# Kernel optimization log

Hardware: AMD Instinct MI355X
Metric: run time of the kernel (lower is better)

## Reference

```python
import jax, jax.numpy as jnp
import numpy as np

S, D, H, E = 4096, 1024, 16, 64  # seq_len, embed_dim, n_heads, head_size


def setup_inputs() -> dict:
    key = jax.random.key(0)
    ks = jax.random.split(key, 8)
    s_d = 1.0 / np.sqrt(D).astype(np.float32)
    return {
        "x": jax.random.normal(ks[0], (S, D), jnp.float32),
        # per-head Q/K/V projections (no bias), stacked over heads: [H, D, E]
        "Wk": jax.random.normal(ks[1], (H, D, E), jnp.float32) * s_d,
        "Wq": jax.random.normal(ks[2], (H, D, E), jnp.float32) * s_d,
        "Wv": jax.random.normal(ks[3], (H, D, E), jnp.float32) * s_d,
        # output projection Dense(D) with bias
        "Wo": jax.random.normal(ks[4], (H * E, D), jnp.float32) * (1.0 / np.sqrt(H * E).astype(np.float32)),
        "bo": jnp.zeros((D,), jnp.float32),
        # MLP: Dense(4D) -> gelu -> Dense(D), both with bias
        "W1": jax.random.normal(ks[5], (D, 4 * D), jnp.float32) * s_d,
        "b1": jnp.zeros((4 * D,), jnp.float32),
        "W2": jax.random.normal(ks[6], (4 * D, D), jnp.float32) * (1.0 / np.sqrt(4 * D).astype(np.float32)),
        "b2": jnp.zeros((D,), jnp.float32),
    }


def _attention(x, Wk, Wq, Wv):
    # per-head projections, vectorized over heads (original loops in Python)
    k = jnp.einsum('sd,hde->hse', x, Wk)
    q = jnp.einsum('sd,hde->hse', x, Wq)
    v = jnp.einsum('sd,hde->hse', x, Wv)
    # NOTE: original computes keys @ queries.T -> scores[i, j] = k_i . q_j
    scores = jnp.einsum('hse,hte->hst', k, q) / jnp.sqrt(jnp.float32(E))
    mask = jnp.tril(jnp.ones((x.shape[0], x.shape[0]), dtype=bool))  # [S, S]
    w = jax.nn.softmax(jnp.where(mask, scores, -jnp.inf), axis=-1)   # [H, S, S]
    out = jnp.einsum('hst,hte->hse', w, v)                            # [H, S, E]
    # concatenate heads along feature axis (head 0 first, matching the loop)
    return out.transpose(1, 0, 2).reshape(x.shape[0], -1)             # [S, H*E]


def reference(x, Wk, Wq, Wv, Wo, bo, W1, b1, W2, b2):
    x = x + _attention(x, Wk, Wq, Wv) @ Wo + bo
    h = jax.nn.gelu(x @ W1 + b1, approximate=True)  # flax default gelu (tanh approx)
    return x + h @ W2 + b2
```

## Files before the change

### kernel.cpp

```cpp
#include <hip/hip_runtime.h>

typedef __attribute__((ext_vector_type(8))) short s16x8;
typedef __attribute__((ext_vector_type(4))) short s16x4;
typedef __attribute__((ext_vector_type(4))) float f32x4;


__device__ __forceinline__ unsigned short f2bf(float f) {
    union { float f; unsigned u; } v; v.f = f;
    unsigned r = v.u + 0x7FFFu + ((v.u >> 16) & 1u);
    return (unsigned short)(r >> 16);
}

__device__ __forceinline__ unsigned cvt_pk_bf16(float lo, float hi) {
    unsigned r;
    asm("v_cvt_pk_bf16_f32 %0, %1, %2" : "=v"(r) : "v"(lo), "v"(hi));
    return r;
}

__device__ __forceinline__ float exp2_fast(float x) {
    float r;
    asm("v_exp_f32 %0, %1" : "=v"(r) : "v"(x));
    return r;
}

__device__ __forceinline__ float gelu_tanh(float x) {
    float u = 0.7978845608028654f * (x + 0.044715f * x * x * x);
    float au = fabsf(u);
    float t = 1.f - 2.f / (__expf(2.f * au) + 1.f);
    t = (u < 0.f) ? -t : t;
    return 0.5f * x * (1.f + t);
}

__device__ __forceinline__ void load_lds16(const void* g, void* l) {
    __builtin_amdgcn_global_load_lds(
        (const __attribute__((address_space(1))) void*)g,
        (__attribute__((address_space(3))) void*)l, 16, 0, 0);
}

__device__ __forceinline__ void xcd_remap(int& bx, int& by) {
    const int gx = gridDim.x;
    const int nwg = gx * gridDim.y;
    const int id = by * gx + bx;
    const int nid = (id & 7) * (nwg >> 3) + (id >> 3);
    bx = nid % gx; by = nid / gx;
}


__global__ void convert_bf16_k(const float* __restrict__ in,
                               unsigned short* __restrict__ out, int n) {
    int i = (blockIdx.x * blockDim.x + threadIdx.x) * 4;
    if (i >= n) return;
    float4 v = *(const float4*)(in + i);
    ushort4 o;
    o.x = f2bf(v.x); o.y = f2bf(v.y); o.z = f2bf(v.z); o.w = f2bf(v.w);
    *(ushort4*)(out + i) = o;
}

__global__ void transpose_k(const float* __restrict__ in,
                            unsigned short* __restrict__ out, int R, int C) {
    __shared__ float tile[32][33];
    const int b = blockIdx.z;
    const int c0 = blockIdx.x * 32, r0 = blockIdx.y * 32;
    const float* inb = in + (size_t)b * R * C;
    unsigned short* outb = out + (size_t)b * R * C;
    const int tx = threadIdx.x, ty = threadIdx.y;
    #pragma unroll
    for (int i = 0; i < 4; ++i)
        tile[ty + i*8][tx] = inb[(size_t)(r0 + ty + i*8) * C + c0 + tx];
    __syncthreads();
    #pragma unroll
    for (int i = 0; i < 4; ++i)
        outb[(size_t)(c0 + ty + i*8) * R + r0 + tx] = f2bf(tile[tx][ty + i*8]);
}

template<int EPI>
__global__ __launch_bounds__(256) void gemm_bt(
    const unsigned short* __restrict__ A,
    const unsigned short* __restrict__ BT,
    const float* __restrict__ bias,
    const float* __restrict__ resid,
    float* __restrict__ Cf,
    unsigned short* __restrict__ Cb,
    int M, int N, int K)
{
    __shared__ unsigned short As[3][128 * 32];
    __shared__ unsigned short Bs[3][128 * 32];
    const int tid = threadIdx.x;
    const int w  = tid >> 6, l = tid & 63;
    const int wr = w >> 1,  wc = w & 1;
    const int lg = l >> 4,  ll = l & 15;
    int bx = blockIdx.x, by = blockIdx.y;
    xcd_remap(bx, by);
    const int m0 = by * 128, n0 = bx * 128;

    const int srow = w * 16 + (l >> 2);
    const int scol = (((l & 3) ^ ((l >> 2) & 3))) * 8;

    f32x4 acc[4][4] = {};

    auto stage = [&](int buf, int k0) {
        #pragma unroll
        for (int i = 0; i < 2; ++i) {
            load_lds16(A  + (size_t)(m0 + srow + i*64) * K + k0 + scol,
                       (char*)As[buf] + i*4096 + w*1024);
            load_lds16(BT + (size_t)(n0 + srow + i*64) * K + k0 + scol,
                       (char*)Bs[buf] + i*4096 + w*1024);
        }
    };

    const int nsteps = K >> 5;
    stage(0, 0); stage(1, 32);
    int buf = 0;
    for (int s = 0; s < nsteps; ++s) {
        if (s + 1 < nsteps) asm volatile("s_waitcnt vmcnt(4)" ::: "memory");
        else                asm volatile("s_waitcnt vmcnt(0)" ::: "memory");
        __builtin_amdgcn_s_barrier();
        s16x8 a[4], b[4];
        #pragma unroll
        for (int m = 0; m < 4; ++m) {
            const int row = wr*64 + m*16 + ll;
            a[m] = *(const s16x8*)&As[buf][row * 32 + ((lg ^ (ll & 3)) * 8)];
        }
        #pragma unroll
        for (int n = 0; n < 4; ++n) {
            const int row = wc*64 + n*16 + ll;
            b[n] = *(const s16x8*)&Bs[buf][row * 32 + ((lg ^ (ll & 3)) * 8)];
        }
        int bnext = buf + 2; if (bnext >= 3) bnext -= 3;
        if (s + 2 < nsteps) stage(bnext, (s + 2) << 5);
        __builtin_amdgcn_s_setprio(1);
        #pragma unroll
        for (int m = 0; m < 4; ++m)
            #pragma unroll
            for (int n = 0; n < 4; ++n)
                acc[m][n] = __builtin_amdgcn_mfma_f32_16x16x32_bf16(a[m], b[n], acc[m][n], 0, 0, 0);
        __builtin_amdgcn_s_setprio(0);
        buf = (buf == 2) ? 0 : buf + 1;
    }

    #pragma unroll
    for (int m = 0; m < 4; ++m) {
        #pragma unroll
        for (int n = 0; n < 4; ++n) {
            const int col = n0 + wc*64 + n*16 + ll;
            #pragma unroll
            for (int r = 0; r < 4; ++r) {
                const int row = m0 + wr*64 + m*16 + lg*4 + r;
                float v = acc[m][n][r];
                if constexpr (EPI == 2) v = gelu_tanh(v + bias[col]);
                if constexpr (EPI == 4) v *= (col < 1024) ? 0.1803368801f : 1.0f;
                Cb[(size_t)row * N + col] = f2bf(v);
            }
        }
    }
}

template<int EPI>
__global__ __launch_bounds__(256) void gemm_bt64(
    const unsigned short* __restrict__ A,
    const unsigned short* __restrict__ BT,
    const float* __restrict__ bias,
    const float* __restrict__ resid,
    float* __restrict__ Cf,
    unsigned short* __restrict__ Cb,
    int M, int N, int K)
{
    __shared__ unsigned short As[4][128 * 32];
    __shared__ unsigned short Bs[4][64 * 32];
    const int tid = threadIdx.x;
    const int w  = tid >> 6, l = tid & 63;
    const int lg = l >> 4,  ll = l & 15;
    int bx = blockIdx.x, by = blockIdx.y;
    xcd_remap(bx, by);
    const int m0 = by * 128, n0 = bx * 64;

    const int srowA = w * 16 + (l >> 2);
    const int scolA = (((l & 3) ^ ((l >> 2) & 3))) * 8;
    const int srowB = tid >> 2;
    const int scolB = (((tid & 3) ^ ((tid >> 2) & 3))) * 8;

    f32x4 acc[2][4] = {};

    auto stage = [&](int buf, int k0) {
        #pragma unroll
        for (int i = 0; i < 2; ++i)
            load_lds16(A + (size_t)(m0 + srowA + i*64) * K + k0 + scolA,
                       (char*)As[buf] + i*4096 + w*1024);
        load_lds16(BT + (size_t)(n0 + srowB) * K + k0 + scolB,
                   (char*)Bs[buf] + w*1024);
    };

    const int nsteps = K >> 5;
    stage(0, 0); stage(1, 32); stage(2, 64);
    int buf = 0;
    for (int s = 0; s < nsteps; ++s) {
        const int rem = nsteps - 1 - s;
        if (rem >= 2)      asm volatile("s_waitcnt vmcnt(6)" ::: "memory");
        else if (rem == 1) asm volatile("s_waitcnt vmcnt(3)" ::: "memory");
        else               asm volatile("s_waitcnt vmcnt(0)" ::: "memory");
        __builtin_amdgcn_s_barrier();
        s16x8 a[2], b[4];
        #pragma unroll
        for (int m = 0; m < 2; ++m) {
            const int row = w*32 + m*16 + ll;
            a[m] = *(const s16x8*)&As[buf][row * 32 + ((lg ^ (ll & 3)) * 8)];
        }
        #pragma unroll
        for (int n = 0; n < 4; ++n) {
            const int row = n*16 + ll;
            b[n] = *(const s16x8*)&Bs[buf][row * 32 + ((lg ^ (ll & 3)) * 8)];
        }
        int bnext = buf + 3; if (bnext >= 4) bnext -= 4;
        if (s + 3 < nsteps) stage(bnext, (s + 3) << 5);
        __builtin_amdgcn_s_setprio(1);
        #pragma unroll
        for (int m = 0; m < 2; ++m)
            #pragma unroll
            for (int n = 0; n < 4; ++n)
                acc[m][n] = __builtin_amdgcn_mfma_f32_16x16x32_bf16(a[m], b[n], acc[m][n], 0, 0, 0);
        __builtin_amdgcn_s_setprio(0);
        buf = (buf + 1) & 3;
    }

    #pragma unroll
    for (int m = 0; m < 2; ++m) {
        #pragma unroll
        for (int n = 0; n < 4; ++n) {
            const int col = n0 + n*16 + ll;
            #pragma unroll
            for (int r = 0; r < 4; ++r) {
                const int row = m0 + w*32 + m*16 + lg*4 + r;
                float v = acc[m][n][r];
                if constexpr (EPI == 1 || EPI == 3) v += bias[col] + resid[(size_t)row * N + col];
                if constexpr (EPI != 3)
                    Cb[(size_t)row * N + col] = f2bf(v);
                if constexpr (EPI == 1 || EPI == 3)
                    Cf[(size_t)row * N + col] = v;
            }
        }
    }
}

__global__ __launch_bounds__(256) void attn_k(
    const unsigned short* __restrict__ Rq,
    const unsigned short* __restrict__ Ck,
    const unsigned short* __restrict__ Vt,
    unsigned short* __restrict__ Out)
{
    __shared__ unsigned short Ks[3][64 * 64];
    __shared__ unsigned short Vs[3][64 * 64];

    const int bx = blockIdx.x;
    const int h  = bx & 15;
    const int sb = 63 - (bx >> 4);
    const int TOTAL = sb + 1;

    const int tid = threadIdx.x;
    const int w = tid >> 6, l = tid & 63;
    const int lg = l >> 4, ll = l & 15;

    const int gsrc  = ((l & 7) ^ (l >> 3)) * 8;
    const int kOff0 = (w*16 +     (l >> 3)) * 2048 + h*64 + gsrc;
    const int kOff1 = (w*16 + 8 + (l >> 3)) * 2048 + h*64 + gsrc;
    const int vOff0 = (h*64 + w*16 +     (l >> 3)) * 4096 + gsrc;
    const int vOff1 = (h*64 + w*16 + 8 + (l >> 3)) * 4096 + gsrc;
    const int ldsOff = w * 2048;

    int qkoff[4][2];
    #pragma unroll
    for (int jj = 0; jj < 4; ++jj) {
        const int row = jj*16 + ll, r7 = row & 7;
        qkoff[jj][0] = row*128 + ((lg)     ^ r7) * 16;
        qkoff[jj][1] = row*128 + ((4 + lg) ^ r7) * 16;
    }
    int pvoff[4][2][2];
    #pragma unroll
    for (int n = 0; n < 4; ++n) {
        const int row = n*16 + ll, r7 = row & 7;
        #pragma unroll
        for (int c = 0; c < 2; ++c) {
            const int gl = (c*4     + (lg >> 1)) ^ r7;
            const int gh = (c*4 + 2 + (lg >> 1)) ^ r7;
            pvoff[n][c][0] = row*128 + gl*16 + (lg & 1)*8;
            pvoff[n][c][1] = row*128 + gh*16 + (lg & 1)*8;
        }
    }

    auto stage = [&](int t, int buf) {
        const unsigned short* qsrc = Ck + (size_t)t * 131072;
        const unsigned short* vsrc = Vt + t * 64;
        char* kd = (char*)Ks[buf] + ldsOff;
        char* vd = (char*)Vs[buf] + ldsOff;
        load_lds16(qsrc + kOff0, kd);
        load_lds16(qsrc + kOff1, kd + 1024);
        load_lds16(vsrc + vOff0, vd);
        load_lds16(vsrc + vOff1, vd + 1024);
    };

    const int qg = sb*64 + w*16 + ll;
    const size_t rb = (size_t)qg * 2048 + h*64;
    const s16x8 r0 = *(const s16x8*)&Rq[rb + lg*8];
    const s16x8 r1 = *(const s16x8*)&Rq[rb + 32 + lg*8];

    const short onebf = (short)0x3F80;
    const s16x8 ones = {onebf, onebf, onebf, onebf, onebf, onebf, onebf, onebf};

    f32x4 o[4] = {};
    f32x4 o4 = {};

    stage(0, 0); stage(1 < TOTAL ? 1 : 0, 1);
    int buf = 0;

    for (int t = 0; t < TOTAL; ++t) {
        if (t < TOTAL-1) asm volatile("s_waitcnt vmcnt(4)" ::: "memory");
        else             asm volatile("s_waitcnt vmcnt(0)" ::: "memory");
        __builtin_amdgcn_s_barrier();
        const char* kb = (const char*)Ks[buf];
        const char* vb = (const char*)Vs[buf];
        const bool diag = (t == TOTAL-1);

        f32x4 st[4];
        __builtin_amdgcn_s_setprio(1);
        #pragma unroll
        for (int jj = 0; jj < 4; ++jj) {
            s16x8 k0 = *(const s16x8*)(kb + qkoff[jj][0]);
            s16x8 k1 = *(const s16x8*)(kb + qkoff[jj][1]);
            f32x4 z = {0.f, 0.f, 0.f, 0.f};
            f32x4 t0 = __builtin_amdgcn_mfma_f32_16x16x32_bf16(k0, r0, z, 0, 0, 0);
            st[jj] = __builtin_amdgcn_mfma_f32_16x16x32_bf16(k1, r1, t0, 0, 0, 0);
        }
        __builtin_amdgcn_s_setprio(0);

        int bnext = buf + 2; if (bnext >= 3) bnext -= 3;
        if (t + 2 < TOTAL) stage(t + 2, bnext);

        float p[4][4];
        if (diag) {
            #pragma unroll
            for (int jj = 0; jj < 4; ++jj)
                #pragma unroll
                for (int r = 0; r < 4; ++r) {
                    const int jg = t*64 + jj*16 + lg*4 + r;
                    p[jj][r] = exp2_fast((jg > qg) ? -3e38f : st[jj][r]);
                }
        } else {
            #pragma unroll
            for (int jj = 0; jj < 4; ++jj)
                #pragma unroll
                for (int r = 0; r < 4; ++r)
                    p[jj][r] = exp2_fast(st[jj][r]);
        }

        s16x8 apv[2];
        #pragma unroll
        for (int c = 0; c < 2; ++c) {
            union { unsigned u[4]; s16x8 v; } pk;
            pk.u[0] = cvt_pk_bf16(p[2*c][0],   p[2*c][1]);
            pk.u[1] = cvt_pk_bf16(p[2*c][2],   p[2*c][3]);
            pk.u[2] = cvt_pk_bf16(p[2*c+1][0], p[2*c+1][1]);
            pk.u[3] = cvt_pk_bf16(p[2*c+1][2], p[2*c+1][3]);
            apv[c] = pk.v;
        }
        __builtin_amdgcn_s_setprio(1);
        o4 = __builtin_amdgcn_mfma_f32_16x16x32_bf16(apv[0], ones, o4, 0, 0, 0);
        o4 = __builtin_amdgcn_mfma_f32_16x16x32_bf16(apv[1], ones, o4, 0, 0, 0);
        #pragma unroll
        for (int n = 0; n < 4; ++n) {
            #pragma unroll
            for (int c = 0; c < 2; ++c) {
                s16x4 lo = *(const s16x4*)(vb + pvoff[n][c][0]);
                s16x4 hi = *(const s16x4*)(vb + pvoff[n][c][1]);
                union { s16x4 h2[2]; s16x8 v; } u;
                u.h2[0] = lo; u.h2[1] = hi;
                o[n] = __builtin_amdgcn_mfma_f32_16x16x32_bf16(apv[c], u.v, o[n], 0, 0, 0);
            }
        }
        __builtin_amdgcn_s_setprio(0);

        buf = (buf == 2) ? 0 : buf + 1;
    }

    #pragma unroll
    for (int r = 0; r < 4; ++r) {
        const float li = 1.f / o4[r];
        const size_t orow = (size_t)(sb*64 + w*16 + lg*4 + r) * 1024 + h * 64;
        #pragma unroll
        for (int n = 0; n < 4; ++n)
            Out[orow + n*16 + ll] = f2bf(o[n][r] * li);
    }
}


extern "C" void kernel_launch(void* const* d_in, const int* in_sizes, int n_in,
                              void* d_out, int out_size, void* d_ws, size_t ws_size,
                              hipStream_t stream) {
    const float* x  = (const float*)d_in[0];
    const float* Wk = (const float*)d_in[1];
    const float* Wq = (const float*)d_in[2];
    const float* Wv = (const float*)d_in[3];
    const float* Wo = (const float*)d_in[4];
    const float* bo = (const float*)d_in[5];
    const float* W1 = (const float*)d_in[6];
    const float* b1 = (const float*)d_in[7];
    const float* W2 = (const float*)d_in[8];
    const float* b2 = (const float*)d_in[9];
    float* out = (float*)d_out;

    char* ws = (char*)d_ws;
    unsigned short* x_bf  = (unsigned short*)(ws);
    unsigned short* WqkT  = (unsigned short*)(ws + (8u  << 20));
    unsigned short* WvT   = (unsigned short*)(ws + (12u << 20));
    unsigned short* WoT   = (unsigned short*)(ws + (14u << 20));
    unsigned short* W1T   = (unsigned short*)(ws + (16u << 20));
    unsigned short* W2T   = (unsigned short*)(ws + (24u << 20));
    unsigned short* QKm   = (unsigned short*)(ws + (32u << 20));
    unsigned short* attn  = (unsigned short*)(ws + (48u << 20));
    unsigned short* Vt    = (unsigned short*)(ws + (56u << 20));
    float*          yf    = (float*)(ws + (64u << 20));
    unsigned short* y_bf  = x_bf;
    unsigned short* h_bf  = QKm;

    dim3 tb(32, 8);
    convert_bf16_k<<<4096, 256, 0, stream>>>(x, x_bf, 4096 * 1024);
    transpose_k<<<dim3(2, 32, 16),  tb, 0, stream>>>(Wq, WqkT,               1024, 64);
    transpose_k<<<dim3(2, 32, 16),  tb, 0, stream>>>(Wk, WqkT + 1024 * 1024, 1024, 64);
    transpose_k<<<dim3(2, 32, 16),  tb, 0, stream>>>(Wv, WvT, 1024, 64);
    transpose_k<<<dim3(32, 32, 1),  tb, 0, stream>>>(Wo, WoT, 1024, 1024);
    transpose_k<<<dim3(128, 32, 1), tb, 0, stream>>>(W1, W1T, 1024, 4096);
    transpose_k<<<dim3(32, 128, 1), tb, 0, stream>>>(W2, W2T, 4096, 1024);

    gemm_bt<4><<<dim3(16, 32), 256, 0, stream>>>(x_bf, WqkT, nullptr, nullptr, nullptr,
                                                 QKm, 4096, 2048, 1024);
    gemm_bt64<0><<<dim3(64, 8), 256, 0, stream>>>(WvT, x_bf, nullptr, nullptr, nullptr,
                                                  Vt, 1024, 4096, 1024);

    attn_k<<<1024, 256, 0, stream>>>(QKm + 1024 , QKm , Vt, attn);

    gemm_bt64<1><<<dim3(16, 32), 256, 0, stream>>>(attn, WoT, bo, x, yf, y_bf, 4096, 1024, 1024);
    gemm_bt<2><<<dim3(32, 32),   256, 0, stream>>>(y_bf, W1T, b1, nullptr, nullptr, h_bf, 4096, 4096, 1024);
    gemm_bt64<3><<<dim3(16, 32), 256, 0, stream>>>(h_bf, W2T, b2, yf, out, nullptr, 4096, 1024, 4096);
}
```

Baseline: 255.7 us.

## Process 128 query rows per attention block, sharing K/V tiles across two row sets

The attention kernel now handles 128 query rows per block, with each wave taking two 16-row sets, instead of 64 rows per block. Every K/V tile staged into LDS therefore feeds twice as many MFMAs, and the grid is halved to 512 blocks. Each tile also covers more of the diagonal, so the last two tiles are masked. This cuts K/V global loads and per-tile barrier overhead, but it doubles accumulator register pressure and gives fewer blocks for load balance across the causal triangle.

```diff
diff --git a/kernel.cpp b/kernel.cpp
--- a/kernel.cpp
+++ b/kernel.cpp
@@ -252,8 +252,8 @@
 
     const int bx = blockIdx.x;
     const int h  = bx & 15;
-    const int sb = 63 - (bx >> 4);
-    const int TOTAL = sb + 1;
+    const int sb = 31 - (bx >> 4);
+    const int TOTAL = 2*sb + 2;
 
     const int tid = threadIdx.x;
     const int w = tid >> 6, l = tid & 63;
@@ -297,18 +297,23 @@
         load_lds16(vsrc + vOff1, vd + 1024);
     };
 
-    const int qg = sb*64 + w*16 + ll;
-    const size_t rb = (size_t)qg * 2048 + h*64;
-    const s16x8 r0 = *(const s16x8*)&Rq[rb + lg*8];
-    const s16x8 r1 = *(const s16x8*)&Rq[rb + 32 + lg*8];
+    const int row0 = sb*128 + w*32;
+    const int qgA  = row0 + ll;
+    const int qgB  = row0 + 16 + ll;
+    const size_t rbA = (size_t)qgA * 2048 + h*64;
+    const size_t rbB = (size_t)qgB * 2048 + h*64;
+    const s16x8 rA0 = *(const s16x8*)&Rq[rbA + lg*8];
+    const s16x8 rA1 = *(const s16x8*)&Rq[rbA + 32 + lg*8];
+    const s16x8 rB0 = *(const s16x8*)&Rq[rbB + lg*8];
+    const s16x8 rB1 = *(const s16x8*)&Rq[rbB + 32 + lg*8];
 
     const short onebf = (short)0x3F80;
     const s16x8 ones = {onebf, onebf, onebf, onebf, onebf, onebf, onebf, onebf};
 
-    f32x4 o[4] = {};
-    f32x4 o4 = {};
-
-    stage(0, 0); stage(1 < TOTAL ? 1 : 0, 1);
+    f32x4 o[2][4] = {};
+    f32x4 o4[2] = {};
+
+    stage(0, 0); stage(1, 1);
     int buf = 0;
 
     for (int t = 0; t < TOTAL; ++t) {
@@ -317,53 +322,63 @@
         __builtin_amdgcn_s_barrier();
         const char* kb = (const char*)Ks[buf];
         const char* vb = (const char*)Vs[buf];
-        const bool diag = (t == TOTAL-1);
-
-        f32x4 st[4];
+        const bool diag = (t >= 2*sb);
+
+        f32x4 st[2][4];
         __builtin_amdgcn_s_setprio(1);
         #pragma unroll
         for (int jj = 0; jj < 4; ++jj) {
             s16x8 k0 = *(const s16x8*)(kb + qkoff[jj][0]);
             s16x8 k1 = *(const s16x8*)(kb + qkoff[jj][1]);
             f32x4 z = {0.f, 0.f, 0.f, 0.f};
-            f32x4 t0 = __builtin_amdgcn_mfma_f32_16x16x32_bf16(k0, r0, z, 0, 0, 0);
-            st[jj] = __builtin_amdgcn_mfma_f32_16x16x32_bf16(k1, r1, t0, 0, 0, 0);
+            f32x4 ta = __builtin_amdgcn_mfma_f32_16x16x32_bf16(k0, rA0, z, 0, 0, 0);
+            st[0][jj] = __builtin_amdgcn_mfma_f32_16x16x32_bf16(k1, rA1, ta, 0, 0, 0);
+            f32x4 tb = __builtin_amdgcn_mfma_f32_16x16x32_bf16(k0, rB0, z, 0, 0, 0);
+            st[1][jj] = __builtin_amdgcn_mfma_f32_16x16x32_bf16(k1, rB1, tb, 0, 0, 0);
         }
         __builtin_amdgcn_s_setprio(0);
 
         int bnext = buf + 2; if (bnext >= 3) bnext -= 3;
         if (t + 2 < TOTAL) stage(t + 2, bnext);
 
-        float p[4][4];
+        float p[2][4][4];
         if (diag) {
             #pragma unroll
             for (int jj = 0; jj < 4; ++jj)
                 #pragma unroll
                 for (int r = 0; r < 4; ++r) {
                     const int jg = t*64 + jj*16 + lg*4 + r;
-                    p[jj][r] = exp2_fast((jg > qg) ? -3e38f : st[jj][r]);
+                    p[0][jj][r] = exp2_fast((jg > qgA) ? -3e38f : st[0][jj][r]);
+                    p[1][jj][r] = exp2_fast((jg > qgB) ? -3e38f : st[1][jj][r]);
                 }
         } else {
             #pragma unroll
-            for (int jj = 0; jj < 4; ++jj)
+            for (int rs = 0; rs < 2; ++rs)
                 #pragma unroll
-                for (int r = 0; r < 4; ++r)
-                    p[jj][r] = exp2_fast(st[jj][r]);
-        }
-
-        s16x8 apv[2];
-        #pragma unroll
-        for (int c = 0; c < 2; ++c) {
-            union { unsigned u[4]; s16x8 v; } pk;
-            pk.u[0] = cvt_pk_bf16(p[2*c][0],   p[2*c][1]);
-            pk.u[1] = cvt_pk_bf16(p[2*c][2],   p[2*c][3]);
-            pk.u[2] = cvt_pk_bf16(p[2*c+1][0], p[2*c+1][1]);
-            pk.u[3] = cvt_pk_bf16(p[2*c+1][2], p[2*c+1][3]);
-            apv[c] = pk.v;
-        }
+                for (int jj = 0; jj < 4; ++jj)
+                    #pragma unroll
+                    for (int r = 0; r < 4; ++r)
+                        p[rs][jj][r] = exp2_fast(st[rs][jj][r]);
+        }
+
+        s16x8 apv[2][2];
+        #pragma unroll
+        for (int rs = 0; rs < 2; ++rs)
+            #pragma unroll
+            for (int c = 0; c < 2; ++c) {
+                union { unsigned u[4]; s16x8 v; } pk;
+                pk.u[0] = cvt_pk_bf16(p[rs][2*c][0],   p[rs][2*c][1]);
+                pk.u[1] = cvt_pk_bf16(p[rs][2*c][2],   p[rs][2*c][3]);
+                pk.u[2] = cvt_pk_bf16(p[rs][2*c+1][0], p[rs][2*c+1][1]);
+                pk.u[3] = cvt_pk_bf16(p[rs][2*c+1][2], p[rs][2*c+1][3]);
+                apv[rs][c] = pk.v;
+            }
         __builtin_amdgcn_s_setprio(1);
-        o4 = __builtin_amdgcn_mfma_f32_16x16x32_bf16(apv[0], ones, o4, 0, 0, 0);
-        o4 = __builtin_amdgcn_mfma_f32_16x16x32_bf16(apv[1], ones, o4, 0, 0, 0);
+        #pragma unroll
+        for (int rs = 0; rs < 2; ++rs) {
+            o4[rs] = __builtin_amdgcn_mfma_f32_16x16x32_bf16(apv[rs][0], ones, o4[rs], 0, 0, 0);
+            o4[rs] = __builtin_amdgcn_mfma_f32_16x16x32_bf16(apv[rs][1], ones, o4[rs], 0, 0, 0);
+        }
         #pragma unroll
         for (int n = 0; n < 4; ++n) {
             #pragma unroll
@@ -372,7 +387,8 @@
                 s16x4 hi = *(const s16x4*)(vb + pvoff[n][c][1]);
                 union { s16x4 h2[2]; s16x8 v; } u;
                 u.h2[0] = lo; u.h2[1] = hi;
-                o[n] = __builtin_amdgcn_mfma_f32_16x16x32_bf16(apv[c], u.v, o[n], 0, 0, 0);
+                o[0][n] = __builtin_amdgcn_mfma_f32_16x16x32_bf16(apv[0][c], u.v, o[0][n], 0, 0, 0);
+                o[1][n] = __builtin_amdgcn_mfma_f32_16x16x32_bf16(apv[1][c], u.v, o[1][n], 0, 0, 0);
             }
         }
         __builtin_amdgcn_s_setprio(0);
@@ -381,13 +397,15 @@
     }
 
     #pragma unroll
-    for (int r = 0; r < 4; ++r) {
-        const float li = 1.f / o4[r];
-        const size_t orow = (size_t)(sb*64 + w*16 + lg*4 + r) * 1024 + h * 64;
-        #pragma unroll
-        for (int n = 0; n < 4; ++n)
-            Out[orow + n*16 + ll] = f2bf(o[n][r] * li);
-    }
+    for (int rs = 0; rs < 2; ++rs)
+        #pragma unroll
+        for (int r = 0; r < 4; ++r) {
+            const float li = 1.f / o4[rs][r];
+            const size_t orow = (size_t)(row0 + rs*16 + lg*4 + r) * 1024 + h * 64;
+            #pragma unroll
+            for (int n = 0; n < 4; ++n)
+                Out[orow + n*16 + ll] = f2bf(o[rs][n][r] * li);
+        }
 }
 
 
@@ -434,7 +452,7 @@
     gemm_bt64<0><<<dim3(64, 8), 256, 0, stream>>>(WvT, x_bf, nullptr, nullptr, nullptr,
                                                   Vt, 1024, 4096, 1024);
 
-    attn_k<<<1024, 256, 0, stream>>>(QKm + 1024 , QKm , Vt, attn);
+    attn_k<<<512, 256, 0, stream>>>(QKm + 1024 , QKm , Vt, attn);
 
     gemm_bt64<1><<<dim3(16, 32), 256, 0, stream>>>(attn, WoT, bo, x, yf, y_bf, 4096, 1024, 1024);
     gemm_bt<2><<<dim3(32, 32),   256, 0, stream>>>(y_bf, W1T, b1, nullptr, nullptr, h_bf, 4096, 4096, 1024);
```

New measurement: 262.3 us. 2.6% more time.
